# Kernel tuning notes

Hardware: AMD Instinct MI355X
Metric: run time of the kernel (lower is better)

Reference implementation:

```python
import jax, jax.numpy as jnp
import numpy as np

B, C2D, C3D, H, W, N = 4, 64, 64, 256, 256, 16384
NEG_SLOPE = 0.1


def _conv1x1_lrelu(x, w, b):
    # 1x1 conv (no norm) + leaky_relu(0.1), per Conv2dNormRelu defaults
    y = jnp.einsum('bchw,oc->bohw', x, w) + b[None, :, None, None]
    return jax.nn.leaky_relu(y, NEG_SLOPE)


def _batch_gather(feat, idx):
    # feat: [B, C, N], idx: [B, P] -> [B, C, P]
    return jnp.take_along_axis(feat, idx[:, None, :], axis=2)


def setup_inputs() -> dict:
    key = jax.random.key(0)
    ks = jax.random.split(key, 14)
    f = jax.random.normal
    s = 0.05
    return {
        'xy': jax.random.uniform(ks[0], (B, 2, N), jnp.float32) * jnp.float32(W),
        'feat_2d': f(ks[1], (B, C2D, H, W), jnp.float32),
        'feat_3d': f(ks[2], (B, C3D, N), jnp.float32),
        'last_flow_2d': f(ks[3], (B, 2, H, W), jnp.float32),
        'last_flow_3d_to_2d': f(ks[4], (B, 2, N), jnp.float32),
        'nn_proj': jax.random.randint(ks[5], (B, H, W, 1), 0, N, jnp.int32),
        'w1': f(ks[6], (C3D, C3D + 5), jnp.float32) * s,
        'b1': f(ks[7], (C3D,), jnp.float32) * s,
        'w2': f(ks[8], (C3D, C3D), jnp.float32) * s,
        'b2': f(ks[9], (C3D,), jnp.float32) * s,
        'w3': f(ks[10], (C3D, C3D), jnp.float32) * s,
        'b3': f(ks[11], (C3D,), jnp.float32) * s,
        'wf': f(ks[12], (C2D, C2D + C3D), jnp.float32) * s,
        'bf': f(ks[13], (C2D,), jnp.float32) * s,
    }


def reference(xy, feat_2d, feat_3d, last_flow_2d, last_flow_3d_to_2d, nn_proj,
              w1, b1, w2, b2, w3, b3, wf, bf):
    b, _, h, w = feat_2d.shape
    # concat per-point flow onto 3D features: [B, C3D+2, N]
    feat_3d_aug = jnp.concatenate([feat_3d, last_flow_3d_to_2d], axis=1)

    idx = nn_proj[..., 0].reshape(b, h * w)  # nearest-neighbor point per pixel
    gathered = _batch_gather(feat_3d_aug, idx).reshape(b, -1, h, w)  # [B, C3D+2, H, W]
    xy_proj = _batch_gather(xy, idx).reshape(b, 2, h, w)             # [B, 2, H, W]

    # pixel-coordinate mesh grid: channel 0 = x (width), channel 1 = y (height)
    gy, gx = jnp.meshgrid(jnp.arange(h, dtype=xy.dtype), jnp.arange(w, dtype=xy.dtype), indexing='ij')
    grid = jnp.stack([gx, gy], axis=0)[None]  # [1, 2, H, W]
    offset = xy_proj - grid                    # [B, 2, H, W]

    # correlation between gathered 3D feats and 2D feats (channel mean)
    corr = jnp.mean(gathered[:, :C2D] * feat_2d, axis=1, keepdims=True)  # [B, 1, H, W]

    # last 2 channels are the projected flow; subtract detached last_flow_2d
    flow_ch = gathered[:, -2:] - jax.lax.stop_gradient(last_flow_2d)
    x = jnp.concatenate([corr, offset, gathered[:, :-2], flow_ch], axis=1)  # [B, C3D+5, H, W]

    x = _conv1x1_lrelu(x, w1, b1)
    x = _conv1x1_lrelu(x, w2, b2)
    x = _conv1x1_lrelu(x, w3, b3)
    out = _conv1x1_lrelu(jnp.concatenate([x, feat_2d], axis=1), wf, bf)  # [B, C2D, H, W]
    return out
```

## Files before the change

kernel.cpp:

```cpp
#include <hip/hip_runtime.h>

#define BB 4
#define CH 64
#define HW 65536
#define NN 16384
#define NT 128
#define XPITCH 104
#define W1OFS 0
#define W2OFS 6144
#define W3OFS 10240
#define WFOFS 14336
#define FWS_BYTE 46080
#define PTAB_BYTE 49152
#define PT_ROW 160
#define WS_NEED ((size_t)PTAB_BYTE + (size_t)BB * NN * PT_ROW)

typedef __attribute__((ext_vector_type(8))) short short8;
typedef __attribute__((ext_vector_type(4))) float f32x4;

union frag_u { unsigned short u[8]; short8 v; };
union row_u  { uint4 q[4]; unsigned short u[32]; };

static __device__ __forceinline__ unsigned short f2bf(float x) {
    unsigned int u = __float_as_uint(x);
    return (unsigned short)((u + 0x7fffu + ((u >> 16) & 1u)) >> 16);
}
static __device__ __forceinline__ float bf2f(unsigned short h) {
    return __uint_as_float(((unsigned int)h) << 16);
}

__global__ __launch_bounds__(256) void prep_w(
    const float* __restrict__ w1, const float* __restrict__ b1,
    const float* __restrict__ w2, const float* __restrict__ b2,
    const float* __restrict__ w3, const float* __restrict__ b3,
    const float* __restrict__ wf, const float* __restrict__ bf,
    unsigned short* __restrict__ wpk, float* __restrict__ fws)
{
    const int t = threadIdx.x;
    for (int i = t; i < 64 * 96; i += 256) {
        const int m = i / 96, k = i % 96;
        float v = 0.f;
        if (k < 64) v = w1[m * 69 + 3 + k];
        else if (k == 64) v = w1[m * 69 + 0];
        else if (k == 67) v = w1[m * 69 + 67];
        else if (k == 68) v = w1[m * 69 + 68];
        wpk[W1OFS + i] = f2bf(v);
    }
    for (int i = t; i < 64 * 64; i += 256) wpk[W2OFS + i] = f2bf(w2[i]);
    for (int i = t; i < 64 * 64; i += 256) wpk[W3OFS + i] = f2bf(w3[i]);
    for (int i = t; i < 64 * 128; i += 256) wpk[WFOFS + i] = f2bf(wf[i]);
    if (t < 64) {
        fws[t]       = b1[t];
        fws[64 + t]  = b2[t];
        fws[128 + t] = b3[t];
        fws[192 + t] = bf[t];
        fws[256 + t] = w1[t * 69 + 1];
        fws[320 + t] = w1[t * 69 + 2];
    }
}

__global__ __launch_bounds__(256) void prep_t(
    const float* __restrict__ xy, const float* __restrict__ f3d,
    const float* __restrict__ lf3d, char* __restrict__ pt)
{
    const int gn = blockIdx.x * 256 + threadIdx.x;
    const int b = blockIdx.y;
    row_u r0, r1;
#pragma unroll
    for (int c = 0; c < 32; c++) r0.u[c] = f2bf(f3d[(size_t)(b * CH + c) * NN + gn]);
#pragma unroll
    for (int c = 0; c < 32; c++) r1.u[c] = f2bf(f3d[(size_t)(b * CH + 32 + c) * NN + gn]);
    char* row = pt + ((size_t)b * NN + gn) * PT_ROW;
    uint4* rq = (uint4*)row;
#pragma unroll
    for (int k = 0; k < 4; k++) rq[k] = r0.q[k];
#pragma unroll
    for (int k = 0; k < 4; k++) rq[4 + k] = r1.q[k];
    float4 e;
    e.x = xy[(size_t)(b * 2 + 0) * NN + gn];
    e.y = xy[(size_t)(b * 2 + 1) * NN + gn];
    e.z = lf3d[(size_t)(b * 2 + 0) * NN + gn];
    e.w = lf3d[(size_t)(b * 2 + 1) * NN + gn];
    *(float4*)(row + 144) = e;
}

template<int KT, int KROW, bool LO>
static __device__ __forceinline__ void layer_mfma(
    const unsigned short* __restrict__ wrow,
    const unsigned short* Xh, const unsigned short* Xl,
    int w, int ln, int q, f32x4 acc[4][2])
{
#pragma unroll
    for (int kt = 0; kt < KT; kt++) {
        const int kcol = kt * 32 + q * 8;
        short8 A[4];
#pragma unroll
        for (int mi = 0; mi < 4; mi++)
            A[mi] = *(const short8*)(wrow + (mi * 16 + ln) * KROW + kcol);
#pragma unroll
        for (int ni = 0; ni < 2; ni++) {
            const int nr = 32 * w + ni * 16 + ln;
            short8 bh = *(const short8*)(Xh + nr * XPITCH + kcol);
            short8 bl = bh;
            if (LO) bl = *(const short8*)(Xl + nr * XPITCH + kcol);
#pragma unroll
            for (int mi = 0; mi < 4; mi++) {
                acc[mi][ni] = __builtin_amdgcn_mfma_f32_16x16x32_bf16(A[mi], bh, acc[mi][ni], 0, 0, 0);
                if (LO)
                    acc[mi][ni] = __builtin_amdgcn_mfma_f32_16x16x32_bf16(A[mi], bl, acc[mi][ni], 0, 0, 0);
            }
        }
    }
}

static __device__ __forceinline__ void zero_acc(f32x4 acc[4][2]) {
#pragma unroll
    for (int mi = 0; mi < 4; mi++)
#pragma unroll
        for (int ni = 0; ni < 2; ni++)
#pragma unroll
            for (int r = 0; r < 4; r++) acc[mi][ni][r] = 0.f;
}

static __device__ __forceinline__ void epi_x(
    f32x4 acc[4][2], const float* __restrict__ fws, int bofs, bool off_fix,
    const float* offsp, unsigned short* Xh, unsigned short* Xl,
    int w, int ln, int q)
{
#pragma unroll
    for (int mi = 0; mi < 4; mi++) {
        const float4 bias = *(const float4*)(fws + bofs + mi * 16 + q * 4);
        float4 wox = bias, woy = bias;
        if (off_fix) {
            wox = *(const float4*)(fws + 256 + mi * 16 + q * 4);
            woy = *(const float4*)(fws + 320 + mi * 16 + q * 4);
        }
#pragma unroll
        for (int ni = 0; ni < 2; ni++) {
            const int nr = 32 * w + ni * 16 + ln;
            float ox = 0.f, oy = 0.f;
            if (off_fix) { ox = offsp[nr]; oy = offsp[NT + nr]; }
            unsigned int hh0 = 0, hh1 = 0, ll0 = 0, ll1 = 0;
#pragma unroll
            for (int r = 0; r < 4; r++) {
                float a = acc[mi][ni][r] + ((const float*)&bias)[r];
                if (off_fix) a += ((const float*)&wox)[r] * ox + ((const float*)&woy)[r] * oy;
                a = fmaxf(a, 0.1f * a);
                const unsigned short hb = f2bf(a);
                const unsigned short lb = f2bf(a - bf2f(hb));
                if (r == 0) { hh0 = hb; ll0 = lb; }
                if (r == 1) { hh0 |= ((unsigned)hb) << 16; ll0 |= ((unsigned)lb) << 16; }
                if (r == 2) { hh1 = hb; ll1 = lb; }
                if (r == 3) { hh1 |= ((unsigned)hb) << 16; ll1 |= ((unsigned)lb) << 16; }
            }
            *(uint2*)&Xh[nr * XPITCH + mi * 16 + q * 4] = make_uint2(hh0, hh1);
            *(uint2*)&Xl[nr * XPITCH + mi * 16 + q * 4] = make_uint2(ll0, ll1);
        }
    }
}

__global__ __launch_bounds__(256, 2) void fuse(
    const float* __restrict__ feat2d, const float* __restrict__ lf2d,
    const int* __restrict__ nn,
    const unsigned short* __restrict__ wpk, const float* __restrict__ fws,
    const char* __restrict__ ptab,
    float* __restrict__ out)
{
    __shared__ unsigned short Xhi[NT * XPITCH];
    __shared__ unsigned short Xlo[NT * XPITCH];
    __shared__ float corrP[2 * NT];
    __shared__ float offsS[2 * NT];
    __shared__ float fcfS[2 * NT];
    __shared__ int idxL[NT];

    const int tid = threadIdx.x;
    const int w = tid >> 6, lane = tid & 63;
    const int q = lane >> 4, ln = lane & 15;
    const int b = blockIdx.y;
    const int p0 = blockIdx.x * NT;

    if (w == 0) {
        idxL[lane] = nn[(size_t)b * HW + p0 + lane];
        idxL[64 + lane] = nn[(size_t)b * HW + p0 + 64 + lane];
    }
    __syncthreads();

    {
        const int h = w >> 1, cp = w & 1;
        const int n = h * 64 + lane;
        const int p = p0 + n;
        const int idx = idxL[n];
        const char* prow = ptab + ((size_t)b * NN + idx) * PT_ROW;
        row_u g;
#pragma unroll
        for (int k = 0; k < 4; k++) g.q[k] = ((const uint4*)prow)[cp * 4 + k];
        float ca = 0.f;
#pragma unroll
        for (int i = 0; i < 32; i++) {
            const int c = cp * 32 + i;
            const float f = feat2d[(size_t)(b * CH + c) * HW + p];
            ca += f * bf2f(g.u[i]);
        }
        corrP[cp * NT + n] = ca;
        uint4* xp = (uint4*)&Xhi[n * XPITCH + cp * 32];
#pragma unroll
        for (int k = 0; k < 4; k++) xp[k] = g.q[k];
        if (cp == 0) {
            const float4 e = *(const float4*)(prow + 144);
            offsS[n] = e.x - (float)(p & 255);
            offsS[NT + n] = e.y - (float)(p >> 8);
            fcfS[n] = e.z - lf2d[(size_t)(b * 2 + 0) * HW + p];
            fcfS[NT + n] = e.w - lf2d[(size_t)(b * 2 + 1) * HW + p];
        }
    }
    __syncthreads();
    if ((w & 1) == 0) {
        const int n = (w >> 1) * 64 + lane;
        const float corr = (corrP[n] + corrP[NT + n]) * (1.0f / 64.0f);
        const unsigned short chh = f2bf(corr);
        const unsigned short xhh = f2bf(fcfS[n]);
        const unsigned short yhh = f2bf(fcfS[NT + n]);
        uint4* tp = (uint4*)&Xhi[n * XPITCH + 64];
        tp[0] = make_uint4((unsigned)chh, ((unsigned)xhh) << 16, (unsigned)yhh, 0u);
        tp[1] = make_uint4(0, 0, 0, 0);
        tp[2] = make_uint4(0, 0, 0, 0);
        tp[3] = make_uint4(0, 0, 0, 0);
    }
    __syncthreads();

    f32x4 acc[4][2];
    zero_acc(acc);
    layer_mfma<3, 96, false>(wpk + W1OFS, Xhi, Xlo, w, ln, q, acc);
    epi_x(acc, fws, 0, true, offsS, Xhi, Xlo, w, ln, q);
    zero_acc(acc);
    layer_mfma<2, 64, true>(wpk + W2OFS, Xhi, Xlo, w, ln, q, acc);
    epi_x(acc, fws, 64, false, offsS, Xhi, Xlo, w, ln, q);
    zero_acc(acc);
    layer_mfma<2, 64, true>(wpk + W3OFS, Xhi, Xlo, w, ln, q, acc);
    epi_x(acc, fws, 128, false, offsS, Xhi, Xlo, w, ln, q);
    zero_acc(acc);
    layer_mfma<2, 128, true>(wpk + WFOFS, Xhi, Xlo, w, ln, q, acc);
#pragma unroll
    for (int kt = 2; kt < 4; kt++) {
        const int kcol = kt * 32 + q * 8;
        short8 A[4];
#pragma unroll
        for (int mi = 0; mi < 4; mi++)
            A[mi] = *(const short8*)(wpk + WFOFS + (mi * 16 + ln) * 128 + kcol);
#pragma unroll
        for (int ni = 0; ni < 2; ni++) {
            frag_u fh;
#pragma unroll
            for (int j = 0; j < 8; j++) {
                const int c = (kt - 2) * 32 + q * 8 + j;
                const float v = feat2d[(size_t)(b * CH + c) * HW + p0 + 32 * w + ni * 16 + ln];
                fh.u[j] = f2bf(v);
            }
#pragma unroll
            for (int mi = 0; mi < 4; mi++)
                acc[mi][ni] = __builtin_amdgcn_mfma_f32_16x16x32_bf16(A[mi], fh.v, acc[mi][ni], 0, 0, 0);
        }
    }
#pragma unroll
    for (int mi = 0; mi < 4; mi++) {
        const float4 bias = *(const float4*)(fws + 192 + mi * 16 + q * 4);
#pragma unroll
        for (int ni = 0; ni < 2; ni++) {
#pragma unroll
            for (int r = 0; r < 4; r++) {
                float a = acc[mi][ni][r] + ((const float*)&bias)[r];
                a = fmaxf(a, 0.1f * a);
                const int m = mi * 16 + q * 4 + r;
                out[(size_t)(b * CH + m) * HW + p0 + 32 * w + ni * 16 + ln] = a;
            }
        }
    }
}

__global__ __launch_bounds__(256) void fuse_slow(
    const float* __restrict__ feat2d, const float* __restrict__ lf2d,
    const float* __restrict__ xy, const float* __restrict__ feat3d,
    const float* __restrict__ lf3d, const int* __restrict__ nn,
    const float* __restrict__ w1, const float* __restrict__ b1,
    const float* __restrict__ w2, const float* __restrict__ b2,
    const float* __restrict__ w3, const float* __restrict__ b3,
    const float* __restrict__ wf, const float* __restrict__ bfv,
    float* __restrict__ out)
{
    const int p = blockIdx.x * 256 + threadIdx.x;
    const int b = blockIdx.y;
    const int idx = nn[(size_t)b * HW + p];
    const float* f3 = feat3d + (size_t)b * CH * NN + idx;
    float g[CH];
#pragma unroll
    for (int c = 0; c < CH; c++) g[c] = f3[(size_t)c * NN];
    const float fl3x = lf3d[(size_t)(b * 2 + 0) * NN + idx];
    const float fl3y = lf3d[(size_t)(b * 2 + 1) * NN + idx];
    const float xyx = xy[(size_t)(b * 2 + 0) * NN + idx];
    const float xyy = xy[(size_t)(b * 2 + 1) * NN + idx];
    const float* f2p = feat2d + (size_t)b * CH * HW + p;
    float corr = 0.f;
#pragma unroll
    for (int c = 0; c < CH; c++) corr += f2p[(size_t)c * HW] * g[c];
    corr *= (1.f / 64.f);
    float xin[69];
    xin[0] = corr;
    xin[1] = xyx - (float)(p & 255);
    xin[2] = xyy - (float)(p >> 8);
#pragma unroll
    for (int c = 0; c < CH; c++) xin[3 + c] = g[c];
    xin[67] = fl3x - lf2d[(size_t)(b * 2 + 0) * HW + p];
    xin[68] = fl3y - lf2d[(size_t)(b * 2 + 1) * HW + p];
    float x1[64], x2[64], x3[64], accv[64];
#pragma unroll
    for (int o = 0; o < 64; o++) {
        float a = b1[o];
#pragma unroll
        for (int k = 0; k < 69; k++) a += w1[o * 69 + k] * xin[k];
        x1[o] = (a >= 0.f) ? a : 0.1f * a;
    }
#pragma unroll
    for (int o = 0; o < 64; o++) {
        float a = b2[o];
#pragma unroll
        for (int k = 0; k < 64; k++) a += w2[o * 64 + k] * x1[k];
        x2[o] = (a >= 0.f) ? a : 0.1f * a;
    }
#pragma unroll
    for (int o = 0; o < 64; o++) {
        float a = b3[o];
#pragma unroll
        for (int k = 0; k < 64; k++) a += w3[o * 64 + k] * x2[k];
        x3[o] = (a >= 0.f) ? a : 0.1f * a;
    }
#pragma unroll
    for (int o = 0; o < 64; o++) {
        float a = bfv[o];
#pragma unroll
        for (int k = 0; k < 64; k++) a += wf[o * 128 + k] * x3[k];
        accv[o] = a;
    }
#pragma unroll
    for (int k = 0; k < 64; k++) {
        const float f = f2p[(size_t)k * HW];
#pragma unroll
        for (int o = 0; o < 64; o++) accv[o] += wf[o * 128 + 64 + k] * f;
    }
#pragma unroll
    for (int o = 0; o < 64; o++) {
        float a = accv[o];
        a = (a >= 0.f) ? a : 0.1f * a;
        out[(size_t)(b * CH + o) * HW + p] = a;
    }
}

extern "C" void kernel_launch(void* const* d_in, const int* in_sizes, int n_in,
                              void* d_out, int out_size, void* d_ws, size_t ws_size,
                              hipStream_t stream)
{
    const float* xy   = (const float*)d_in[0];
    const float* f2d  = (const float*)d_in[1];
    const float* f3d  = (const float*)d_in[2];
    const float* lf2d = (const float*)d_in[3];
    const float* lf3d = (const float*)d_in[4];
    const int*   nn   = (const int*)d_in[5];
    const float* w1 = (const float*)d_in[6];
    const float* b1 = (const float*)d_in[7];
    const float* w2 = (const float*)d_in[8];
    const float* b2 = (const float*)d_in[9];
    const float* w3 = (const float*)d_in[10];
    const float* b3 = (const float*)d_in[11];
    const float* wf = (const float*)d_in[12];
    const float* bf = (const float*)d_in[13];

    if (ws_size >= WS_NEED) {
        unsigned short* wpk = (unsigned short*)d_ws;
        float* fws = (float*)((char*)d_ws + FWS_BYTE);
        char* pt = (char*)d_ws + PTAB_BYTE;
        prep_w<<<1, 256, 0, stream>>>(w1, b1, w2, b2, w3, b3, wf, bf, wpk, fws);
        prep_t<<<dim3(NN / 256, BB), 256, 0, stream>>>(xy, f3d, lf3d, pt);
        fuse<<<dim3(HW / NT, BB), 256, 0, stream>>>(f2d, lf2d, nn, wpk, fws, pt, (float*)d_out);
    } else {
        fuse_slow<<<dim3(HW / 256, BB), 256, 0, stream>>>(f2d, lf2d, xy, f3d, lf3d, nn,
                                                          w1, b1, w2, b2, w3, b3, wf, bf,
                                                          (float*)d_out);
    }
}
```

Baseline: 248.2 us.

## Double fuse block to 512 threads and split prep kernels across more blocks

The main fused kernel now runs 8 waves per 128-pixel tile, each owning 16 pixel rows instead of 32, and the gather/correlation stage splits channels four ways instead of two. The weight-packing prep runs on five blocks instead of one, and the point-table prep assigns a quarter of the channels per wave across four times as many blocks. The aim is more latency hiding and parallelism from extra waves per CU. In exchange each wave loads the A weight fragments for fewer MFMAs, so weight reuse per wave drops and LDS weight traffic rises.

```diff
diff --git a/kernel.cpp b/kernel.cpp
--- a/kernel.cpp
+++ b/kernel.cpp
@@ -19,7 +19,7 @@
 typedef __attribute__((ext_vector_type(4))) float f32x4;
 
 union frag_u { unsigned short u[8]; short8 v; };
-union row_u  { uint4 q[4]; unsigned short u[32]; };
+union half_u { uint4 q[2]; unsigned short u[16]; };
 
 static __device__ __forceinline__ unsigned short f2bf(float x) {
     unsigned int u = __float_as_uint(x);
@@ -37,19 +37,24 @@
     unsigned short* __restrict__ wpk, float* __restrict__ fws)
 {
     const int t = threadIdx.x;
-    for (int i = t; i < 64 * 96; i += 256) {
-        const int m = i / 96, k = i % 96;
-        float v = 0.f;
-        if (k < 64) v = w1[m * 69 + 3 + k];
-        else if (k == 64) v = w1[m * 69 + 0];
-        else if (k == 67) v = w1[m * 69 + 67];
-        else if (k == 68) v = w1[m * 69 + 68];
-        wpk[W1OFS + i] = f2bf(v);
-    }
-    for (int i = t; i < 64 * 64; i += 256) wpk[W2OFS + i] = f2bf(w2[i]);
-    for (int i = t; i < 64 * 64; i += 256) wpk[W3OFS + i] = f2bf(w3[i]);
-    for (int i = t; i < 64 * 128; i += 256) wpk[WFOFS + i] = f2bf(wf[i]);
-    if (t < 64) {
+    const int blk = blockIdx.x;
+    if (blk == 0) {
+        for (int i = t; i < 64 * 96; i += 256) {
+            const int m = i / 96, k = i % 96;
+            float v = 0.f;
+            if (k < 64) v = w1[m * 69 + 3 + k];
+            else if (k == 64) v = w1[m * 69 + 0];
+            else if (k == 67) v = w1[m * 69 + 67];
+            else if (k == 68) v = w1[m * 69 + 68];
+            wpk[W1OFS + i] = f2bf(v);
+        }
+    } else if (blk == 1) {
+        for (int i = t; i < 64 * 64; i += 256) wpk[W2OFS + i] = f2bf(w2[i]);
+    } else if (blk == 2) {
+        for (int i = t; i < 64 * 64; i += 256) wpk[W3OFS + i] = f2bf(w3[i]);
+    } else if (blk == 3) {
+        for (int i = t; i < 64 * 128; i += 256) wpk[WFOFS + i] = f2bf(wf[i]);
+    } else if (t < 64) {
         fws[t]       = b1[t];
         fws[64 + t]  = b2[t];
         fws[128 + t] = b3[t];
@@ -63,32 +68,34 @@
     const float* __restrict__ xy, const float* __restrict__ f3d,
     const float* __restrict__ lf3d, char* __restrict__ pt)
 {
-    const int gn = blockIdx.x * 256 + threadIdx.x;
+    const int t = threadIdx.x;
+    const int cq = t >> 6;
+    const int l = t & 63;
+    const int gn = blockIdx.x * 64 + l;
     const int b = blockIdx.y;
-    row_u r0, r1;
-#pragma unroll
-    for (int c = 0; c < 32; c++) r0.u[c] = f2bf(f3d[(size_t)(b * CH + c) * NN + gn]);
-#pragma unroll
-    for (int c = 0; c < 32; c++) r1.u[c] = f2bf(f3d[(size_t)(b * CH + 32 + c) * NN + gn]);
+    half_u r;
+#pragma unroll
+    for (int i = 0; i < 16; i++)
+        r.u[i] = f2bf(f3d[(size_t)(b * CH + cq * 16 + i) * NN + gn]);
     char* row = pt + ((size_t)b * NN + gn) * PT_ROW;
     uint4* rq = (uint4*)row;
-#pragma unroll
-    for (int k = 0; k < 4; k++) rq[k] = r0.q[k];
-#pragma unroll
-    for (int k = 0; k < 4; k++) rq[4 + k] = r1.q[k];
-    float4 e;
-    e.x = xy[(size_t)(b * 2 + 0) * NN + gn];
-    e.y = xy[(size_t)(b * 2 + 1) * NN + gn];
-    e.z = lf3d[(size_t)(b * 2 + 0) * NN + gn];
-    e.w = lf3d[(size_t)(b * 2 + 1) * NN + gn];
-    *(float4*)(row + 144) = e;
+    rq[2 * cq] = r.q[0];
+    rq[2 * cq + 1] = r.q[1];
+    if (cq == 0) {
+        float4 e;
+        e.x = xy[(size_t)(b * 2 + 0) * NN + gn];
+        e.y = xy[(size_t)(b * 2 + 1) * NN + gn];
+        e.z = lf3d[(size_t)(b * 2 + 0) * NN + gn];
+        e.w = lf3d[(size_t)(b * 2 + 1) * NN + gn];
+        *(float4*)(row + 144) = e;
+    }
 }
 
 template<int KT, int KROW, bool LO>
 static __device__ __forceinline__ void layer_mfma(
     const unsigned short* __restrict__ wrow,
     const unsigned short* Xh, const unsigned short* Xl,
-    int w, int ln, int q, f32x4 acc[4][2])
+    int rowb, int ln, int q, f32x4 acc[4])
 {
 #pragma unroll
     for (int kt = 0; kt < KT; kt++) {
@@ -97,36 +104,34 @@
 #pragma unroll
         for (int mi = 0; mi < 4; mi++)
             A[mi] = *(const short8*)(wrow + (mi * 16 + ln) * KROW + kcol);
-#pragma unroll
-        for (int ni = 0; ni < 2; ni++) {
-            const int nr = 32 * w + ni * 16 + ln;
-            short8 bh = *(const short8*)(Xh + nr * XPITCH + kcol);
-            short8 bl = bh;
-            if (LO) bl = *(const short8*)(Xl + nr * XPITCH + kcol);
-#pragma unroll
-            for (int mi = 0; mi < 4; mi++) {
-                acc[mi][ni] = __builtin_amdgcn_mfma_f32_16x16x32_bf16(A[mi], bh, acc[mi][ni], 0, 0, 0);
-                if (LO)
-                    acc[mi][ni] = __builtin_amdgcn_mfma_f32_16x16x32_bf16(A[mi], bl, acc[mi][ni], 0, 0, 0);
-            }
-        }
-    }
-}
-
-static __device__ __forceinline__ void zero_acc(f32x4 acc[4][2]) {
+        const int nr = rowb + ln;
+        short8 bh = *(const short8*)(Xh + nr * XPITCH + kcol);
+        short8 bl = bh;
+        if (LO) bl = *(const short8*)(Xl + nr * XPITCH + kcol);
+#pragma unroll
+        for (int mi = 0; mi < 4; mi++) {
+            acc[mi] = __builtin_amdgcn_mfma_f32_16x16x32_bf16(A[mi], bh, acc[mi], 0, 0, 0);
+            if (LO)
+                acc[mi] = __builtin_amdgcn_mfma_f32_16x16x32_bf16(A[mi], bl, acc[mi], 0, 0, 0);
+        }
+    }
+}
+
+static __device__ __forceinline__ void zero_acc(f32x4 acc[4]) {
 #pragma unroll
     for (int mi = 0; mi < 4; mi++)
 #pragma unroll
-        for (int ni = 0; ni < 2; ni++)
-#pragma unroll
-            for (int r = 0; r < 4; r++) acc[mi][ni][r] = 0.f;
+        for (int r = 0; r < 4; r++) acc[mi][r] = 0.f;
 }
 
 static __device__ __forceinline__ void epi_x(
-    f32x4 acc[4][2], const float* __restrict__ fws, int bofs, bool off_fix,
+    f32x4 acc[4], const float* __restrict__ fws, int bofs, bool off_fix,
     const float* offsp, unsigned short* Xh, unsigned short* Xl,
-    int w, int ln, int q)
-{
+    int rowb, int ln, int q)
+{
+    const int nr = rowb + ln;
+    float ox = 0.f, oy = 0.f;
+    if (off_fix) { ox = offsp[nr]; oy = offsp[NT + nr]; }
 #pragma unroll
     for (int mi = 0; mi < 4; mi++) {
         const float4 bias = *(const float4*)(fws + bofs + mi * 16 + q * 4);
@@ -135,31 +140,25 @@
             wox = *(const float4*)(fws + 256 + mi * 16 + q * 4);
             woy = *(const float4*)(fws + 320 + mi * 16 + q * 4);
         }
-#pragma unroll
-        for (int ni = 0; ni < 2; ni++) {
-            const int nr = 32 * w + ni * 16 + ln;
-            float ox = 0.f, oy = 0.f;
-            if (off_fix) { ox = offsp[nr]; oy = offsp[NT + nr]; }
-            unsigned int hh0 = 0, hh1 = 0, ll0 = 0, ll1 = 0;
-#pragma unroll
-            for (int r = 0; r < 4; r++) {
-                float a = acc[mi][ni][r] + ((const float*)&bias)[r];
-                if (off_fix) a += ((const float*)&wox)[r] * ox + ((const float*)&woy)[r] * oy;
-                a = fmaxf(a, 0.1f * a);
-                const unsigned short hb = f2bf(a);
-                const unsigned short lb = f2bf(a - bf2f(hb));
-                if (r == 0) { hh0 = hb; ll0 = lb; }
-                if (r == 1) { hh0 |= ((unsigned)hb) << 16; ll0 |= ((unsigned)lb) << 16; }
-                if (r == 2) { hh1 = hb; ll1 = lb; }
-                if (r == 3) { hh1 |= ((unsigned)hb) << 16; ll1 |= ((unsigned)lb) << 16; }
-            }
-            *(uint2*)&Xh[nr * XPITCH + mi * 16 + q * 4] = make_uint2(hh0, hh1);
-            *(uint2*)&Xl[nr * XPITCH + mi * 16 + q * 4] = make_uint2(ll0, ll1);
-        }
-    }
-}
-
-__global__ __launch_bounds__(256, 2) void fuse(
+        unsigned int hh0 = 0, hh1 = 0, ll0 = 0, ll1 = 0;
+#pragma unroll
+        for (int r = 0; r < 4; r++) {
+            float a = acc[mi][r] + ((const float*)&bias)[r];
+            if (off_fix) a += ((const float*)&wox)[r] * ox + ((const float*)&woy)[r] * oy;
+            a = fmaxf(a, 0.1f * a);
+            const unsigned short hb = f2bf(a);
+            const unsigned short lb = f2bf(a - bf2f(hb));
+            if (r == 0) { hh0 = hb; ll0 = lb; }
+            if (r == 1) { hh0 |= ((unsigned)hb) << 16; ll0 |= ((unsigned)lb) << 16; }
+            if (r == 2) { hh1 = hb; ll1 = lb; }
+            if (r == 3) { hh1 |= ((unsigned)hb) << 16; ll1 |= ((unsigned)lb) << 16; }
+        }
+        *(uint2*)&Xh[nr * XPITCH + mi * 16 + q * 4] = make_uint2(hh0, hh1);
+        *(uint2*)&Xl[nr * XPITCH + mi * 16 + q * 4] = make_uint2(ll0, ll1);
+    }
+}
+
+__global__ __launch_bounds__(512, 4) void fuse(
     const float* __restrict__ feat2d, const float* __restrict__ lf2d,
     const int* __restrict__ nn,
     const unsigned short* __restrict__ wpk, const float* __restrict__ fws,
@@ -168,7 +167,7 @@
 {
     __shared__ unsigned short Xhi[NT * XPITCH];
     __shared__ unsigned short Xlo[NT * XPITCH];
-    __shared__ float corrP[2 * NT];
+    __shared__ float corrP[4 * NT];
     __shared__ float offsS[2 * NT];
     __shared__ float fcfS[2 * NT];
     __shared__ int idxL[NT];
@@ -178,34 +177,32 @@
     const int q = lane >> 4, ln = lane & 15;
     const int b = blockIdx.y;
     const int p0 = blockIdx.x * NT;
-
-    if (w == 0) {
-        idxL[lane] = nn[(size_t)b * HW + p0 + lane];
-        idxL[64 + lane] = nn[(size_t)b * HW + p0 + 64 + lane];
-    }
+    const int rowb = 16 * w;
+
+    if (tid < NT) idxL[tid] = nn[(size_t)b * HW + p0 + tid];
     __syncthreads();
 
     {
-        const int h = w >> 1, cp = w & 1;
-        const int n = h * 64 + lane;
+        const int cq = w & 3;
+        const int n = (w >> 2) * 64 + lane;
         const int p = p0 + n;
         const int idx = idxL[n];
         const char* prow = ptab + ((size_t)b * NN + idx) * PT_ROW;
-        row_u g;
-#pragma unroll
-        for (int k = 0; k < 4; k++) g.q[k] = ((const uint4*)prow)[cp * 4 + k];
+        half_u g;
+        g.q[0] = ((const uint4*)prow)[2 * cq];
+        g.q[1] = ((const uint4*)prow)[2 * cq + 1];
         float ca = 0.f;
 #pragma unroll
-        for (int i = 0; i < 32; i++) {
-            const int c = cp * 32 + i;
+        for (int i = 0; i < 16; i++) {
+            const int c = cq * 16 + i;
             const float f = feat2d[(size_t)(b * CH + c) * HW + p];
             ca += f * bf2f(g.u[i]);
         }
-        corrP[cp * NT + n] = ca;
-        uint4* xp = (uint4*)&Xhi[n * XPITCH + cp * 32];
-#pragma unroll
-        for (int k = 0; k < 4; k++) xp[k] = g.q[k];
-        if (cp == 0) {
+        corrP[cq * NT + n] = ca;
+        uint4* xp = (uint4*)&Xhi[n * XPITCH + cq * 16];
+        xp[0] = g.q[0];
+        xp[1] = g.q[1];
+        if (cq == 0) {
             const float4 e = *(const float4*)(prow + 144);
             offsS[n] = e.x - (float)(p & 255);
             offsS[NT + n] = e.y - (float)(p >> 8);
@@ -214,9 +211,9 @@
         }
     }
     __syncthreads();
-    if ((w & 1) == 0) {
-        const int n = (w >> 1) * 64 + lane;
-        const float corr = (corrP[n] + corrP[NT + n]) * (1.0f / 64.0f);
+    if (w < 2) {
+        const int n = w * 64 + lane;
+        const float corr = (corrP[n] + corrP[NT + n] + corrP[2 * NT + n] + corrP[3 * NT + n]) * (1.0f / 64.0f);
         const unsigned short chh = f2bf(corr);
         const unsigned short xhh = f2bf(fcfS[n]);
         const unsigned short yhh = f2bf(fcfS[NT + n]);
@@ -228,18 +225,18 @@
     }
     __syncthreads();
 
-    f32x4 acc[4][2];
+    f32x4 acc[4];
     zero_acc(acc);
-    layer_mfma<3, 96, false>(wpk + W1OFS, Xhi, Xlo, w, ln, q, acc);
-    epi_x(acc, fws, 0, true, offsS, Xhi, Xlo, w, ln, q);
+    layer_mfma<3, 96, false>(wpk + W1OFS, Xhi, Xlo, rowb, ln, q, acc);
+    epi_x(acc, fws, 0, true, offsS, Xhi, Xlo, rowb, ln, q);
     zero_acc(acc);
-    layer_mfma<2, 64, true>(wpk + W2OFS, Xhi, Xlo, w, ln, q, acc);
-    epi_x(acc, fws, 64, false, offsS, Xhi, Xlo, w, ln, q);
+    layer_mfma<2, 64, true>(wpk + W2OFS, Xhi, Xlo, rowb, ln, q, acc);
+    epi_x(acc, fws, 64, false, offsS, Xhi, Xlo, rowb, ln, q);
     zero_acc(acc);
-    layer_mfma<2, 64, true>(wpk + W3OFS, Xhi, Xlo, w, ln, q, acc);
-    epi_x(acc, fws, 128, false, offsS, Xhi, Xlo, w, ln, q);
+    layer_mfma<2, 64, true>(wpk + W3OFS, Xhi, Xlo, rowb, ln, q, acc);
+    epi_x(acc, fws, 128, false, offsS, Xhi, Xlo, rowb, ln, q);
     zero_acc(acc);
-    layer_mfma<2, 128, true>(wpk + WFOFS, Xhi, Xlo, w, ln, q, acc);
+    layer_mfma<2, 128, true>(wpk + WFOFS, Xhi, Xlo, rowb, ln, q, acc);
 #pragma unroll
     for (int kt = 2; kt < 4; kt++) {
         const int kcol = kt * 32 + q * 8;
@@ -247,32 +244,26 @@
 #pragma unroll
         for (int mi = 0; mi < 4; mi++)
             A[mi] = *(const short8*)(wpk + WFOFS + (mi * 16 + ln) * 128 + kcol);
-#pragma unroll
-        for (int ni = 0; ni < 2; ni++) {
-            frag_u fh;
-#pragma unroll
-            for (int j = 0; j < 8; j++) {
-                const int c = (kt - 2) * 32 + q * 8 + j;
-                const float v = feat2d[(size_t)(b * CH + c) * HW + p0 + 32 * w + ni * 16 + ln];
-                fh.u[j] = f2bf(v);
-            }
-#pragma unroll
-            for (int mi = 0; mi < 4; mi++)
-                acc[mi][ni] = __builtin_amdgcn_mfma_f32_16x16x32_bf16(A[mi], fh.v, acc[mi][ni], 0, 0, 0);
-        }
+        frag_u fh;
+#pragma unroll
+        for (int j = 0; j < 8; j++) {
+            const int c = (kt - 2) * 32 + q * 8 + j;
+            const float v = feat2d[(size_t)(b * CH + c) * HW + p0 + rowb + ln];
+            fh.u[j] = f2bf(v);
+        }
+#pragma unroll
+        for (int mi = 0; mi < 4; mi++)
+            acc[mi] = __builtin_amdgcn_mfma_f32_16x16x32_bf16(A[mi], fh.v, acc[mi], 0, 0, 0);
     }
 #pragma unroll
     for (int mi = 0; mi < 4; mi++) {
         const float4 bias = *(const float4*)(fws + 192 + mi * 16 + q * 4);
 #pragma unroll
-        for (int ni = 0; ni < 2; ni++) {
-#pragma unroll
-            for (int r = 0; r < 4; r++) {
-                float a = acc[mi][ni][r] + ((const float*)&bias)[r];
-                a = fmaxf(a, 0.1f * a);
-                const int m = mi * 16 + q * 4 + r;
-                out[(size_t)(b * CH + m) * HW + p0 + 32 * w + ni * 16 + ln] = a;
-            }
+        for (int r = 0; r < 4; r++) {
+            float a = acc[mi][r] + ((const float*)&bias)[r];
+            a = fmaxf(a, 0.1f * a);
+            const int m = mi * 16 + q * 4 + r;
+            out[(size_t)(b * CH + m) * HW + p0 + rowb + ln] = a;
         }
     }
 }
@@ -377,9 +368,9 @@
         unsigned short* wpk = (unsigned short*)d_ws;
         float* fws = (float*)((char*)d_ws + FWS_BYTE);
         char* pt = (char*)d_ws + PTAB_BYTE;
-        prep_w<<<1, 256, 0, stream>>>(w1, b1, w2, b2, w3, b3, wf, bf, wpk, fws);
-        prep_t<<<dim3(NN / 256, BB), 256, 0, stream>>>(xy, f3d, lf3d, pt);
-        fuse<<<dim3(HW / NT, BB), 256, 0, stream>>>(f2d, lf2d, nn, wpk, fws, pt, (float*)d_out);
+        prep_w<<<dim3(5), 256, 0, stream>>>(w1, b1, w2, b2, w3, b3, wf, bf, wpk, fws);
+        prep_t<<<dim3(NN / 64, BB), 256, 0, stream>>>(xy, f3d, lf3d, pt);
+        fuse<<<dim3(HW / NT, BB), 512, 0, stream>>>(f2d, lf2d, nn, wpk, fws, pt, (float*)d_out);
     } else {
         fuse_slow<<<dim3(HW / 256, BB), 256, 0, stream>>>(f2d, lf2d, xy, f3d, lf3d, nn,
                                                           w1, b1, w2, b2, w3, b3, wf, bf,
```

Measured after the change: 265.2 us. 6.8% more time.

## Shrink LDS, drop block barriers in fuse, and parallelize the prep kernels

Applied to the files above, without the earlier changes.

The fused kernel now keeps each pixel row within a single wave. Idx loading, the correlation reduction (via a cross-lane shuffle) and the extra-channel packing are all done per wave, so the staging arrays and three __syncthreads are removed. The low-part activation buffer uses a tighter pitch, which lowers LDS per block, and launch bounds are raised to allow three blocks per CU. The weight prep and point-table prep kernels are split across more blocks and threads to cut their serial latency. The tighter register budget from the higher occupancy target risks spills in the MFMA layers.

```diff
diff --git a/kernel.cpp b/kernel.cpp
--- a/kernel.cpp
+++ b/kernel.cpp
@@ -6,6 +6,7 @@
 #define NN 16384
 #define NT 128
 #define XPITCH 104
+#define LPITCH 72
 #define W1OFS 0
 #define W2OFS 6144
 #define W3OFS 10240
@@ -20,6 +21,7 @@
 
 union frag_u { unsigned short u[8]; short8 v; };
 union row_u  { uint4 q[4]; unsigned short u[32]; };
+union half_u { uint4 q[2]; unsigned short u[16]; };
 
 static __device__ __forceinline__ unsigned short f2bf(float x) {
     unsigned int u = __float_as_uint(x);
@@ -37,19 +39,24 @@
     unsigned short* __restrict__ wpk, float* __restrict__ fws)
 {
     const int t = threadIdx.x;
-    for (int i = t; i < 64 * 96; i += 256) {
-        const int m = i / 96, k = i % 96;
-        float v = 0.f;
-        if (k < 64) v = w1[m * 69 + 3 + k];
-        else if (k == 64) v = w1[m * 69 + 0];
-        else if (k == 67) v = w1[m * 69 + 67];
-        else if (k == 68) v = w1[m * 69 + 68];
-        wpk[W1OFS + i] = f2bf(v);
-    }
-    for (int i = t; i < 64 * 64; i += 256) wpk[W2OFS + i] = f2bf(w2[i]);
-    for (int i = t; i < 64 * 64; i += 256) wpk[W3OFS + i] = f2bf(w3[i]);
-    for (int i = t; i < 64 * 128; i += 256) wpk[WFOFS + i] = f2bf(wf[i]);
-    if (t < 64) {
+    const int blk = blockIdx.x;
+    if (blk == 0) {
+        for (int i = t; i < 64 * 96; i += 256) {
+            const int m = i / 96, k = i % 96;
+            float v = 0.f;
+            if (k < 64) v = w1[m * 69 + 3 + k];
+            else if (k == 64) v = w1[m * 69 + 0];
+            else if (k == 67) v = w1[m * 69 + 67];
+            else if (k == 68) v = w1[m * 69 + 68];
+            wpk[W1OFS + i] = f2bf(v);
+        }
+    } else if (blk == 1) {
+        for (int i = t; i < 64 * 64; i += 256) wpk[W2OFS + i] = f2bf(w2[i]);
+    } else if (blk == 2) {
+        for (int i = t; i < 64 * 64; i += 256) wpk[W3OFS + i] = f2bf(w3[i]);
+    } else if (blk == 3) {
+        for (int i = t; i < 64 * 128; i += 256) wpk[WFOFS + i] = f2bf(wf[i]);
+    } else if (t < 64) {
         fws[t]       = b1[t];
         fws[64 + t]  = b2[t];
         fws[128 + t] = b3[t];
@@ -63,25 +70,27 @@
     const float* __restrict__ xy, const float* __restrict__ f3d,
     const float* __restrict__ lf3d, char* __restrict__ pt)
 {
-    const int gn = blockIdx.x * 256 + threadIdx.x;
+    const int t = threadIdx.x;
+    const int cq = t >> 6;
+    const int l = t & 63;
+    const int gn = blockIdx.x * 64 + l;
     const int b = blockIdx.y;
-    row_u r0, r1;
-#pragma unroll
-    for (int c = 0; c < 32; c++) r0.u[c] = f2bf(f3d[(size_t)(b * CH + c) * NN + gn]);
-#pragma unroll
-    for (int c = 0; c < 32; c++) r1.u[c] = f2bf(f3d[(size_t)(b * CH + 32 + c) * NN + gn]);
+    half_u r;
+#pragma unroll
+    for (int i = 0; i < 16; i++)
+        r.u[i] = f2bf(f3d[(size_t)(b * CH + cq * 16 + i) * NN + gn]);
     char* row = pt + ((size_t)b * NN + gn) * PT_ROW;
     uint4* rq = (uint4*)row;
-#pragma unroll
-    for (int k = 0; k < 4; k++) rq[k] = r0.q[k];
-#pragma unroll
-    for (int k = 0; k < 4; k++) rq[4 + k] = r1.q[k];
-    float4 e;
-    e.x = xy[(size_t)(b * 2 + 0) * NN + gn];
-    e.y = xy[(size_t)(b * 2 + 1) * NN + gn];
-    e.z = lf3d[(size_t)(b * 2 + 0) * NN + gn];
-    e.w = lf3d[(size_t)(b * 2 + 1) * NN + gn];
-    *(float4*)(row + 144) = e;
+    rq[2 * cq] = r.q[0];
+    rq[2 * cq + 1] = r.q[1];
+    if (cq == 0) {
+        float4 e;
+        e.x = xy[(size_t)(b * 2 + 0) * NN + gn];
+        e.y = xy[(size_t)(b * 2 + 1) * NN + gn];
+        e.z = lf3d[(size_t)(b * 2 + 0) * NN + gn];
+        e.w = lf3d[(size_t)(b * 2 + 1) * NN + gn];
+        *(float4*)(row + 144) = e;
+    }
 }
 
 template<int KT, int KROW, bool LO>
@@ -102,7 +111,7 @@
             const int nr = 32 * w + ni * 16 + ln;
             short8 bh = *(const short8*)(Xh + nr * XPITCH + kcol);
             short8 bl = bh;
-            if (LO) bl = *(const short8*)(Xl + nr * XPITCH + kcol);
+            if (LO) bl = *(const short8*)(Xl + nr * LPITCH + kcol);
 #pragma unroll
             for (int mi = 0; mi < 4; mi++) {
                 acc[mi][ni] = __builtin_amdgcn_mfma_f32_16x16x32_bf16(A[mi], bh, acc[mi][ni], 0, 0, 0);
@@ -154,12 +163,12 @@
                 if (r == 3) { hh1 |= ((unsigned)hb) << 16; ll1 |= ((unsigned)lb) << 16; }
             }
             *(uint2*)&Xh[nr * XPITCH + mi * 16 + q * 4] = make_uint2(hh0, hh1);
-            *(uint2*)&Xl[nr * XPITCH + mi * 16 + q * 4] = make_uint2(ll0, ll1);
-        }
-    }
-}
-
-__global__ __launch_bounds__(256, 2) void fuse(
+            *(uint2*)&Xl[nr * LPITCH + mi * 16 + q * 4] = make_uint2(ll0, ll1);
+        }
+    }
+}
+
+__global__ __launch_bounds__(256, 3) void fuse(
     const float* __restrict__ feat2d, const float* __restrict__ lf2d,
     const int* __restrict__ nn,
     const unsigned short* __restrict__ wpk, const float* __restrict__ fws,
@@ -167,11 +176,8 @@
     float* __restrict__ out)
 {
     __shared__ unsigned short Xhi[NT * XPITCH];
-    __shared__ unsigned short Xlo[NT * XPITCH];
-    __shared__ float corrP[2 * NT];
+    __shared__ unsigned short Xlo[NT * LPITCH];
     __shared__ float offsS[2 * NT];
-    __shared__ float fcfS[2 * NT];
-    __shared__ int idxL[NT];
 
     const int tid = threadIdx.x;
     const int w = tid >> 6, lane = tid & 63;
@@ -179,17 +185,11 @@
     const int b = blockIdx.y;
     const int p0 = blockIdx.x * NT;
 
-    if (w == 0) {
-        idxL[lane] = nn[(size_t)b * HW + p0 + lane];
-        idxL[64 + lane] = nn[(size_t)b * HW + p0 + 64 + lane];
-    }
-    __syncthreads();
-
     {
-        const int h = w >> 1, cp = w & 1;
-        const int n = h * 64 + lane;
+        const int cp = lane >> 5, j = lane & 31;
+        const int n = 32 * w + j;
         const int p = p0 + n;
-        const int idx = idxL[n];
+        const int idx = nn[(size_t)b * HW + p];
         const char* prow = ptab + ((size_t)b * NN + idx) * PT_ROW;
         row_u g;
 #pragma unroll
@@ -198,35 +198,28 @@
 #pragma unroll
         for (int i = 0; i < 32; i++) {
             const int c = cp * 32 + i;
-            const float f = feat2d[(size_t)(b * CH + c) * HW + p];
-            ca += f * bf2f(g.u[i]);
-        }
-        corrP[cp * NT + n] = ca;
+            ca += feat2d[(size_t)(b * CH + c) * HW + p] * bf2f(g.u[i]);
+        }
         uint4* xp = (uint4*)&Xhi[n * XPITCH + cp * 32];
 #pragma unroll
         for (int k = 0; k < 4; k++) xp[k] = g.q[k];
+        ca += __shfl_xor(ca, 32);
         if (cp == 0) {
             const float4 e = *(const float4*)(prow + 144);
             offsS[n] = e.x - (float)(p & 255);
             offsS[NT + n] = e.y - (float)(p >> 8);
-            fcfS[n] = e.z - lf2d[(size_t)(b * 2 + 0) * HW + p];
-            fcfS[NT + n] = e.w - lf2d[(size_t)(b * 2 + 1) * HW + p];
-        }
-    }
-    __syncthreads();
-    if ((w & 1) == 0) {
-        const int n = (w >> 1) * 64 + lane;
-        const float corr = (corrP[n] + corrP[NT + n]) * (1.0f / 64.0f);
-        const unsigned short chh = f2bf(corr);
-        const unsigned short xhh = f2bf(fcfS[n]);
-        const unsigned short yhh = f2bf(fcfS[NT + n]);
-        uint4* tp = (uint4*)&Xhi[n * XPITCH + 64];
-        tp[0] = make_uint4((unsigned)chh, ((unsigned)xhh) << 16, (unsigned)yhh, 0u);
-        tp[1] = make_uint4(0, 0, 0, 0);
-        tp[2] = make_uint4(0, 0, 0, 0);
-        tp[3] = make_uint4(0, 0, 0, 0);
-    }
-    __syncthreads();
+            const float fcx = e.z - lf2d[(size_t)(b * 2 + 0) * HW + p];
+            const float fcy = e.w - lf2d[(size_t)(b * 2 + 1) * HW + p];
+            const unsigned short chh = f2bf(ca * (1.0f / 64.0f));
+            const unsigned short xhh = f2bf(fcx);
+            const unsigned short yhh = f2bf(fcy);
+            uint4* tp = (uint4*)&Xhi[n * XPITCH + 64];
+            tp[0] = make_uint4((unsigned)chh, ((unsigned)xhh) << 16, (unsigned)yhh, 0u);
+            tp[1] = make_uint4(0, 0, 0, 0);
+            tp[2] = make_uint4(0, 0, 0, 0);
+            tp[3] = make_uint4(0, 0, 0, 0);
+        }
+    }
 
     f32x4 acc[4][2];
     zero_acc(acc);
@@ -377,8 +370,8 @@
         unsigned short* wpk = (unsigned short*)d_ws;
         float* fws = (float*)((char*)d_ws + FWS_BYTE);
         char* pt = (char*)d_ws + PTAB_BYTE;
-        prep_w<<<1, 256, 0, stream>>>(w1, b1, w2, b2, w3, b3, wf, bf, wpk, fws);
-        prep_t<<<dim3(NN / 256, BB), 256, 0, stream>>>(xy, f3d, lf3d, pt);
+        prep_w<<<dim3(5), 256, 0, stream>>>(w1, b1, w2, b2, w3, b3, wf, bf, wpk, fws);
+        prep_t<<<dim3(NN / 64, BB), 256, 0, stream>>>(xy, f3d, lf3d, pt);
         fuse<<<dim3(HW / NT, BB), 256, 0, stream>>>(f2d, lf2d, nn, wpk, fws, pt, (float*)d_out);
     } else {
         fuse_slow<<<dim3(HW / 256, BB), 256, 0, stream>>>(f2d, lf2d, xy, f3d, lf3d, nn,
```

Measured after the change: 237.4 us. 1.05x faster.
